# Kernel tuning notes

Measured on AMD Instinct MI355X. Metric: run time of the kernel, lower is better.

Reference implementation:

```python
import jax, jax.numpy as jnp
import numpy as np

N, E, F_IN, G = 50000, 800000, 128, 256
LAYERS = [(128, 4, 64), (256, 4, 64), (256, 1, 64)]  # (fan_in, heads, per-head dim)


def setup_inputs() -> dict:
    key = jax.random.key(0)
    ks = iter(jax.random.split(key, 64))
    nrm = lambda shp, s=1.0: jax.random.normal(next(ks), shp, jnp.float32) * s
    d = {}
    d["x"] = nrm((N, F_IN))
    d["edge_index"] = jax.random.randint(next(ks), (2, E), 0, N, dtype=jnp.int32)
    d["batch"] = jnp.sort(jax.random.randint(next(ks), (N,), 0, G, dtype=jnp.int32))
    for i, (fin, h, c) in enumerate(LAYERS):
        d[f"w{i}"] = nrm((fin, h * c), 1.0 / np.sqrt(fin))
        d[f"asrc{i}"] = nrm((h, c), 0.1)
        d[f"adst{i}"] = nrm((h, c), 0.1)
        d[f"b{i}"] = nrm((h * c,), 0.1)
        d[f"g{i}"] = 1.0 + nrm((h * c,), 0.1)
        d[f"be{i}"] = nrm((h * c,), 0.1)
        d[f"m{i}"] = nrm((h * c,), 0.1)
        d[f"v{i}"] = jnp.abs(nrm((h * c,), 0.1)) + 1.0
    d["fc1w"] = nrm((192, 64), 1.0 / np.sqrt(192)); d["fc1b"] = nrm((64,), 0.1)
    d["fc2w"] = nrm((64, 32), 1.0 / np.sqrt(64));   d["fc2b"] = nrm((32,), 0.1)
    d["fc3w"] = nrm((32, 1), 1.0 / np.sqrt(32));    d["fc3b"] = nrm((1,), 0.1)
    return d


def _gat_layer(x, w, a_s, a_d, b, src, dst, n, heads):
    c = w.shape[1] // heads
    h = (x @ w).reshape(n, heads, c)                      # [N,H,C]
    al_s = jnp.sum(h * a_s[None], axis=-1)                # [N,H]
    al_d = jnp.sum(h * a_d[None], axis=-1)                # [N,H]
    e = jax.nn.leaky_relu(al_s[src] + al_d[dst], 0.2)     # [E',H]
    emax = jax.ops.segment_max(e, dst, num_segments=n)
    emax = jnp.where(jnp.isfinite(emax), emax, 0.0)
    ee = jnp.exp(e - emax[dst])
    den = jax.ops.segment_sum(ee, dst, num_segments=n)
    alpha = ee / (den[dst] + 1e-16)                       # edge softmax per dst node
    out = jax.ops.segment_sum(h[src] * alpha[..., None], dst, num_segments=n)
    return out.reshape(n, heads * c) + b


def _bn(x, g, be, m, v):
    return (x - m) * jax.lax.rsqrt(v + 1e-5) * g + be


def reference(x, edge_index, batch,
              w0, asrc0, adst0, b0, g0, be0, m0, v0,
              w1, asrc1, adst1, b1, g1, be1, m1, v1,
              w2, asrc2, adst2, b2, g2, be2, m2, v2,
              fc1w, fc1b, fc2w, fc2b, fc3w, fc3b):
    n = x.shape[0]
    loop = jnp.arange(n, dtype=edge_index.dtype)          # add_self_loops (PyG default)
    src = jnp.concatenate([edge_index[0], loop])
    dst = jnp.concatenate([edge_index[1], loop])
    layers = [(w0, asrc0, adst0, b0, g0, be0, m0, v0, 4),
              (w1, asrc1, adst1, b1, g1, be1, m1, v1, 4),
              (w2, asrc2, adst2, b2, g2, be2, m2, v2, 1)]
    for (w, a_s, a_d, b, g, be, m, v, heads) in layers:
        x = _gat_layer(x, w, a_s, a_d, b, src, dst, n, heads)
        x = jax.nn.elu(_bn(x, g, be, m, v))
    # multi-pool readout over graphs
    xsum = jax.ops.segment_sum(x, batch, num_segments=G)
    cnt = jax.ops.segment_sum(jnp.ones((n, 1), x.dtype), batch, num_segments=G)
    xmean = xsum / jnp.maximum(cnt, 1.0)
    xmax = jax.ops.segment_max(x, batch, num_segments=G)
    xmax = jnp.where(jnp.isfinite(xmax), xmax, 0.0)
    h = jnp.concatenate([xmean, xmax, xsum], axis=1)      # [G, 192]
    h = jax.nn.relu(h @ fc1w + fc1b)
    h = jax.nn.relu(h @ fc2w + fc2b)
    return h @ fc3w + fc3b                                # [G, 1]
```

## Files before the change

kernel.cpp:

```cpp
#include <hip/hip_runtime.h>
#include <hip/hip_fp16.h>

typedef unsigned short ushort_t;
typedef unsigned int uint_t;
typedef __attribute__((ext_vector_type(8))) _Float16 half8;
typedef __attribute__((ext_vector_type(4))) float f32x4;

#define NN 50000
#define NE 800000
#define NGR 256
#define MAXDEG 64

typedef __attribute__((address_space(3))) unsigned int as3_u32;
typedef const __attribute__((address_space(1))) unsigned int as1_u32c;
__device__ __forceinline__ void gld16(const ushort_t* g, void* lds_base) {
    __builtin_amdgcn_global_load_lds((as1_u32c*)g, (as3_u32*)lds_base, 16, 0, 0);
}

__global__ void k_prep(const float* __restrict__ x0, __half* __restrict__ xf,
                       const float* __restrict__ W0, const float* __restrict__ W1,
                       const float* __restrict__ W2, __half* __restrict__ th,
                       int* __restrict__ colv, int* __restrict__ deg) {
    int i = blockIdx.x * 256 + threadIdx.x;
    if (i < 1600000) {
        float4 v = ((const float4*)x0)[i];
        __half2 a = __floats2half2_rn(v.x, v.y);
        __half2 b = __floats2half2_rn(v.z, v.w);
        *(__half2*)(xf + i * 4) = a;
        *(__half2*)(xf + i * 4 + 2) = b;
    } else if (i < 1600000 + 114688) {
        int w = i - 1600000;
        const float* W; int K, NC, idx, base;
        if (w < 32768)      { W = W0; K = 128; NC = 256; idx = w;         base = 0; }
        else if (w < 98304) { W = W1; K = 256; NC = 256; idx = w - 32768; base = 32768; }
        else                { W = W2; K = 256; NC = 64;  idx = w - 98304; base = 98304; }
        int k = idx / NC, n = idx % NC;
        th[base + n * K + k] = __float2half(W[idx]);
    } else if (i < 1600000 + 114688 + NN) {
        int n = i - 1714688;
        colv[n << 6] = n;
        deg[n] = 1;
    }
}

template<int KD, int BN>
__device__ __forceinline__ void gemm_body(int bx, int by,
    const __half* __restrict__ Ax, const __half* __restrict__ Bth,
    __half* __restrict__ Hout, const float* __restrict__ a_s,
    const float* __restrict__ a_d, float* __restrict__ als,
    float* __restrict__ ald, int H, int M, int NC) {
    constexpr int BM = 128, BK = 32;
    __shared__ ushort_t sA[BM * BK];
    __shared__ ushort_t sB[BN * BK];
    const int tid = threadIdx.x;
    const int m0 = bx * BM;
    const int n0 = by * BN;
    const int wv = tid >> 6, ln = tid & 63;
    const int lrow = ln & 15, lq = ln >> 4;
    constexpr int RT = (BN == 128) ? 4 : 2;
    int wm, wn;
    if constexpr (BN == 128) { wm = (wv >> 1) * 64; wn = (wv & 1) * 64; }
    else                     { wm = wv * 32;        wn = 0; }
    const int roff = ln >> 2;
    const int coff = (ln & 3) * 8;

    f32x4 acc[RT][4] = {};

    for (int k0 = 0; k0 < KD; k0 += BK) {
        #pragma unroll
        for (int ch = 0; ch < 2; ++ch) {
            int rb = wv * 32 + ch * 16;
            size_t ga = (size_t)(m0 + rb + roff) * KD + k0 + coff;
            gld16((const ushort_t*)Ax + ga, &sA[rb * BK]);
        }
        if constexpr (BN == 128) {
            #pragma unroll
            for (int ch = 0; ch < 2; ++ch) {
                int rb = wv * 32 + ch * 16;
                size_t gb = (size_t)(n0 + rb + roff) * KD + k0 + coff;
                gld16((const ushort_t*)Bth + gb, &sB[rb * BK]);
            }
        } else {
            int rb = wv * 16;
            size_t gb = (size_t)(n0 + rb + roff) * KD + k0 + coff;
            gld16((const ushort_t*)Bth + gb, &sB[rb * BK]);
        }
        __syncthreads();
        half8 af[RT], bf[4];
        #pragma unroll
        for (int r = 0; r < RT; ++r)
            af[r] = *(const half8*)&sA[(wm + r * 16 + lrow) * BK + lq * 8];
        #pragma unroll
        for (int c = 0; c < 4; ++c)
            bf[c] = *(const half8*)&sB[(wn + c * 16 + lrow) * BK + lq * 8];
        #pragma unroll
        for (int r = 0; r < RT; ++r)
            #pragma unroll
            for (int c = 0; c < 4; ++c)
                acc[r][c] = __builtin_amdgcn_mfma_f32_16x16x32_f16(af[r], bf[c], acc[r][c], 0, 0, 0);
        __syncthreads();
    }
    #pragma unroll
    for (int r = 0; r < RT; ++r) {
        #pragma unroll
        for (int c = 0; c < 4; ++c) {
            int colg = n0 + wn + c * 16 + lrow;
            #pragma unroll
            for (int j = 0; j < 4; ++j) {
                int row = m0 + wm + r * 16 + lq * 4 + j;
                if (row < M) Hout[(size_t)row * NC + colg] = __float2half(acc[r][c][j]);
            }
        }
    }
    int hh = (n0 + wn) >> 6;
    float asv[4], adv[4];
    #pragma unroll
    for (int c = 0; c < 4; ++c) {
        int cg = (n0 + wn + c * 16 + lrow) & 63;
        asv[c] = a_s[hh * 64 + cg];
        adv[c] = a_d[hh * 64 + cg];
    }
    #pragma unroll
    for (int r = 0; r < RT; ++r) {
        #pragma unroll
        for (int j = 0; j < 4; ++j) {
            float ts = 0.f, td = 0.f;
            #pragma unroll
            for (int c = 0; c < 4; ++c) {
                float v = acc[r][c][j];
                ts += v * asv[c];
                td += v * adv[c];
            }
            #pragma unroll
            for (int m = 1; m < 16; m <<= 1) {
                ts += __shfl_xor(ts, m);
                td += __shfl_xor(td, m);
            }
            int row = m0 + wm + r * 16 + lq * 4 + j;
            if (lrow == 0 && row < M) {
                als[row * H + hh] = ts;
                ald[row * H + hh] = td;
            }
        }
    }
}

template<int KD, int BN>
__global__ __launch_bounds__(256)
void k_mgemm(const __half* __restrict__ Ax, const __half* __restrict__ Bth,
             __half* __restrict__ Hout,
             const float* __restrict__ a_s, const float* __restrict__ a_d,
             float* __restrict__ als, float* __restrict__ ald,
             int H, int M, int NC) {
    gemm_body<KD, BN>(blockIdx.x, blockIdx.y, Ax, Bth, Hout, a_s, a_d, als, ald, H, M, NC);
}

__global__ __launch_bounds__(256)
void k_gf(const __half* __restrict__ Ax, const __half* __restrict__ Bth,
          __half* __restrict__ Hout,
          const float* __restrict__ a_s, const float* __restrict__ a_d,
          float* __restrict__ als, float* __restrict__ ald, int M,
          const int* __restrict__ esrc, const int* __restrict__ edst,
          int* __restrict__ deg, int* __restrict__ colv) {
    if (blockIdx.x < 782) {
        gemm_body<128, 128>(blockIdx.x >> 1, blockIdx.x & 1, Ax, Bth, Hout,
                            a_s, a_d, als, ald, 4, M, 256);
    } else {
        int fid = blockIdx.x - 782;
        int r = blockIdx.x & 7;
        int c = fid >> 3;
        int base = c * 1024 + (int)threadIdx.x * 4;
        if (base < NE) {
            int4 dv = *(const int4*)(edst + base);
            int4 sv = *(const int4*)(esrc + base);
            const int lo = r * 6250;
            const int* dp = (const int*)&dv;
            const int* sp = (const int*)&sv;
            #pragma unroll
            for (int j = 0; j < 4; ++j) {
                int d = dp[j];
                if ((unsigned)(d - lo) < 6250u) {
                    int pos = atomicAdd(&deg[d], 1);
                    if (pos < MAXDEG) colv[(d << 6) + pos] = sp[j];
                }
            }
        }
    }
}

__global__ __launch_bounds__(256)
void k_fagg4s(const __half* __restrict__ h, const float* __restrict__ als,
              const float* __restrict__ ald, const int* __restrict__ deg,
              const int* __restrict__ colv,
              const float* __restrict__ bias, const float* __restrict__ gam,
              const float* __restrict__ bet, const float* __restrict__ mu,
              const float* __restrict__ var,
              __half* __restrict__ xo, int M) {
    __shared__ uint_t wraw[4][64];
    int wv = threadIdx.x >> 6;
    int half = blockIdx.x & 1;
    int node = (blockIdx.x >> 1) * 4 + wv;
    if (node >= M) return;
    int l = threadIdx.x & 63;
    int dg = deg[node];
    int rs = node << 6;

    float2 ad = *(const float2*)(ald + (size_t)node * 4 + half * 2);
    bool vld = l < dg;
    int s = colv[vld ? rs + l : rs];
    int cv = s;
    float2 av = *(const float2*)((const char*)als + ((size_t)(uint_t)s << 4) + half * 8);
    float e0 = av.x + ad.x; e0 = e0 > 0.f ? e0 : 0.2f * e0; e0 = vld ? __expf(e0) : 0.f;
    float e1 = av.y + ad.y; e1 = e1 > 0.f ? e1 : 0.2f * e1; e1 = vld ? __expf(e1) : 0.f;
    float d0 = e0, d1 = e1;
    __half2 p = __floats2half2_rn(e0, e1);
    wraw[wv][l] = *(uint_t*)&p;
    #pragma unroll
    for (int off = 1; off < 64; off <<= 1) {
        d0 += __shfl_xor(d0, off); d1 += __shfl_xor(d1, off);
    }

    float a0 = 0.f, a1 = 0.f;
    const uint_t shB = (uint_t)((l & 32) >> 1);
    const uint_t loffB = (uint_t)(half * 256 + l * 4);
    int nrem = dg;
    #pragma unroll
    for (int grp = 0; grp < 3; ++grp) {
        int g0 = grp * 24;
        if (g0 < nrem) {
            uint_t hu[3][8];
            #pragma unroll
            for (int bb = 0; bb < 3; ++bb) {
                if (g0 + bb * 8 < nrem) {
                    #pragma unroll
                    for (int u = 0; u < 8; ++u) {
                        int sv = __builtin_amdgcn_readlane(cv, g0 + bb * 8 + u);
                        const char* hp = (const char*)h + ((size_t)(uint_t)sv << 9);
                        hu[bb][u] = *(const uint_t*)(hp + loffB);
                    }
                }
            }
            #pragma unroll
            for (int bb = 0; bb < 3; ++bb) {
                if (g0 + bb * 8 < nrem) {
                    #pragma unroll
                    for (int u = 0; u < 8; ++u) {
                        int j = g0 + bb * 8 + u;
                        uint_t w = wraw[wv][j];
                        uint_t afv = w >> shB;
                        asm("v_fma_mix_f32 %0, %1, %2, %0 op_sel:[0,0,0] op_sel_hi:[1,1,0]"
                            : "+v"(a0) : "v"(afv), "v"(hu[bb][u]));
                        asm("v_fma_mix_f32 %0, %1, %2, %0 op_sel:[0,1,0] op_sel_hi:[1,1,0]"
                            : "+v"(a1) : "v"(afv), "v"(hu[bb][u]));
                    }
                }
            }
        }
    }

    float den = (l & 32) ? d1 : d0;
    float inv = 1.f / (den + 1e-16f);
    int chg = half * 128 + l * 2;
    float2 bi = *(const float2*)(bias + chg);
    float2 ga = *(const float2*)(gam + chg);
    float2 be = *(const float2*)(bet + chg);
    float2 m2 = *(const float2*)(mu + chg);
    float2 v2 = *(const float2*)(var + chg);
    float o0 = a0 * inv + bi.x;
    float o1 = a1 * inv + bi.y;
    float bn0 = (o0 - m2.x) * rsqrtf(v2.x + 1e-5f) * ga.x + be.x;
    float bn1 = (o1 - m2.y) * rsqrtf(v2.y + 1e-5f) * ga.y + be.y;
    float f0 = bn0 > 0.f ? bn0 : (__expf(bn0) - 1.f);
    float f1 = bn1 > 0.f ? bn1 : (__expf(bn1) - 1.f);
    __half2 pk = __floats2half2_rn(f0, f1);
    *(uint_t*)&xo[(size_t)node * 256 + chg] = *(uint_t*)&pk;
}

__global__ __launch_bounds__(256)
void k_fagg1(const __half* __restrict__ h, const float* __restrict__ als,
             const float* __restrict__ ald, const int* __restrict__ deg,
             const int* __restrict__ colv,
             const float* __restrict__ bias, const float* __restrict__ gam,
             const float* __restrict__ bet, const float* __restrict__ mu,
             const float* __restrict__ var,
             float* __restrict__ xf, int M) {
    __shared__ uint_t wraw[4][64];
    int node = blockIdx.x * 4 + (threadIdx.x >> 6);
    if (node >= M) return;
    int wv = (threadIdx.x >> 6) & 3;
    int l = threadIdx.x & 63;
    int dg = deg[node];
    int rs = node << 6;

    float ad = ald[node];
    bool vld = l < dg;
    int s = colv[vld ? rs + l : rs];
    int cv = s;
    float e = als[s] + ad; e = e > 0.f ? e : 0.2f * e; e = vld ? __expf(e) : 0.f;
    float d0 = e;
    wraw[wv][l] = __float_as_uint(e);
    #pragma unroll
    for (int off = 1; off < 64; off <<= 1) d0 += __shfl_xor(d0, off);

    float a0 = 0.f;
    int nrem = dg;
    #pragma unroll
    for (int grp = 0; grp < 3; ++grp) {
        int g0 = grp * 24;
        if (g0 < nrem) {
            uint_t hu[3][8];
            #pragma unroll
            for (int bb = 0; bb < 3; ++bb) {
                if (g0 + bb * 8 < nrem) {
                    #pragma unroll
                    for (int u = 0; u < 8; ++u) {
                        int sv = __builtin_amdgcn_readlane(cv, g0 + bb * 8 + u);
                        const ushort_t* hp = (const ushort_t*)h + ((size_t)(uint_t)sv << 6);
                        hu[bb][u] = (uint_t)hp[l];
                    }
                }
            }
            #pragma unroll
            for (int bb = 0; bb < 3; ++bb) {
                if (g0 + bb * 8 < nrem) {
                    #pragma unroll
                    for (int u = 0; u < 8; ++u) {
                        int j = g0 + bb * 8 + u;
                        uint_t wfv = wraw[wv][j];
                        asm("v_fma_mix_f32 %0, %1, %2, %0 op_sel:[0,0,0] op_sel_hi:[0,1,0]"
                            : "+v"(a0) : "v"(wfv), "v"(hu[bb][u]));
                    }
                }
            }
        }
    }

    float inv = 1.f / (d0 + 1e-16f);
    float o = a0 * inv + bias[l];
    float bn = (o - mu[l]) * rsqrtf(var[l] + 1e-5f) * gam[l] + bet[l];
    float fo = bn > 0.f ? bn : (__expf(bn) - 1.f);
    xf[(size_t)node * 64 + l] = fo;
}

__global__ __launch_bounds__(512)
void k_poolfc(const float* __restrict__ x, const int* __restrict__ batch,
              const float* __restrict__ fc1w, const float* __restrict__ fc1b,
              const float* __restrict__ fc2w, const float* __restrict__ fc2b,
              const float* __restrict__ fc3w, const float* __restrict__ fc3b,
              float* __restrict__ out, int M) {
    __shared__ float ssum[8][64];
    __shared__ float smax[8][64];
    __shared__ float hb[192];
    __shared__ float h1[64];
    __shared__ float h2[32];
    int g = blockIdx.x, t = threadIdx.x;
    int d = t & 63, sub = t >> 6;
    int lo = 0, hi = M;
    while (lo < hi) { int mid = (lo + hi) >> 1; if (batch[mid] < g) lo = mid + 1; else hi = mid; }
    int s = lo;
    lo = 0; hi = M;
    while (lo < hi) { int mid = (lo + hi) >> 1; if (batch[mid] < g + 1) lo = mid + 1; else hi = mid; }
    int e = lo;
    float sum = 0.f, mx = -3.0e38f;
    for (int n = s + sub; n < e; n += 8) {
        float v = x[(size_t)n * 64 + d];
        sum += v; mx = fmaxf(mx, v);
    }
    ssum[sub][d] = sum; smax[sub][d] = mx;
    __syncthreads();
    if (t < 64) {
        float sm = 0.f, m2 = -3.0e38f;
        #pragma unroll
        for (int k = 0; k < 8; ++k) { sm += ssum[k][t]; m2 = fmaxf(m2, smax[k][t]); }
        int cnt = e - s;
        hb[t] = sm / (float)(cnt > 1 ? cnt : 1);
        hb[64 + t] = (cnt == 0) ? 0.f : m2;
        hb[128 + t] = sm;
    }
    __syncthreads();
    if (t < 64) {
        float s1 = fc1b[t];
        for (int k = 0; k < 192; ++k) s1 += hb[k] * fc1w[k * 64 + t];
        h1[t] = fmaxf(s1, 0.f);
    }
    __syncthreads();
    if (t < 32) {
        float s2 = fc2b[t];
        for (int k = 0; k < 64; ++k) s2 += h1[k] * fc2w[k * 32 + t];
        h2[t] = fmaxf(s2, 0.f);
    }
    __syncthreads();
    if (t == 0) {
        float s3 = fc3b[0];
        for (int k = 0; k < 32; ++k) s3 += h2[k] * fc3w[k];
        out[g] = s3;
    }
}

extern "C" void kernel_launch(void* const* d_in, const int* in_sizes, int n_in,
                              void* d_out, int out_size, void* d_ws, size_t ws_size,
                              hipStream_t stream) {
    const float* x0     = (const float*)d_in[0];
    const int* ei       = (const int*)d_in[1];
    const int* batch    = (const int*)d_in[2];
    const float* W[3]   = {(const float*)d_in[3],  (const float*)d_in[11], (const float*)d_in[19]};
    const float* AS[3]  = {(const float*)d_in[4],  (const float*)d_in[12], (const float*)d_in[20]};
    const float* AD[3]  = {(const float*)d_in[5],  (const float*)d_in[13], (const float*)d_in[21]};
    const float* BI[3]  = {(const float*)d_in[6],  (const float*)d_in[14], (const float*)d_in[22]};
    const float* GA[3]  = {(const float*)d_in[7],  (const float*)d_in[15], (const float*)d_in[23]};
    const float* BE[3]  = {(const float*)d_in[8],  (const float*)d_in[16], (const float*)d_in[24]};
    const float* MU[3]  = {(const float*)d_in[9],  (const float*)d_in[17], (const float*)d_in[25]};
    const float* VA[3]  = {(const float*)d_in[10], (const float*)d_in[18], (const float*)d_in[26]};
    const float* fc1w = (const float*)d_in[27];
    const float* fc1b = (const float*)d_in[28];
    const float* fc2w = (const float*)d_in[29];
    const float* fc2b = (const float*)d_in[30];
    const float* fc3w = (const float*)d_in[31];
    const float* fc3b = (const float*)d_in[32];

    char* ws = (char*)d_ws;
    int*   colv   = (int*)  (ws);
    int*   deg    = (int*)  (ws + 12800000);
    float* als    = (float*)(ws + 13000192);
    float* ald    = (float*)(ws + 13800192);
    __half* wTh   = (__half*)(ws + 14600192);
    __half* h_buf = (__half*)(ws + 14829568);
    __half* xf16  = (__half*)(ws + 40429568);
    float* xpool  = (float*)(ws + 66054144);

    const int* esrc = ei;
    const int* edst = ei + NE;

    k_prep<<<(1600000 + 114688 + NN + 255) / 256, 256, 0, stream>>>(x0, xf16, W[0], W[1], W[2],
                                                                    wTh, colv, deg);

    const int GB = (NN + 127) / 128;
    const int FILLB = ((NE + 1023) / 1024) * 8;
    int nwb = (NN + 3) / 4;
    int nsb = nwb * 2;

    k_gf<<<782 + FILLB, 256, 0, stream>>>(xf16, wTh, h_buf, AS[0], AD[0], als, ald, NN,
                                          esrc, edst, deg, colv);
    k_fagg4s<<<nsb, 256, 0, stream>>>(h_buf, als, ald, deg, colv,
                                      BI[0], GA[0], BE[0], MU[0], VA[0], xf16, NN);
    k_mgemm<256, 128><<<dim3(GB, 2), 256, 0, stream>>>(xf16, wTh + 32768, h_buf,
                                                       AS[1], AD[1], als, ald, 4, NN, 256);
    k_fagg4s<<<nsb, 256, 0, stream>>>(h_buf, als, ald, deg, colv,
                                      BI[1], GA[1], BE[1], MU[1], VA[1], xf16, NN);
    k_mgemm<256, 64><<<dim3(GB, 1), 256, 0, stream>>>(xf16, wTh + 98304, h_buf,
                                                      AS[2], AD[2], als, ald, 1, NN, 64);
    k_fagg1<<<nwb, 256, 0, stream>>>(h_buf, als, ald, deg, colv,
                                     BI[2], GA[2], BE[2], MU[2], VA[2], xpool, NN);

    k_poolfc<<<NGR, 512, 0, stream>>>(xpool, batch, fc1w, fc1b, fc2w, fc2b, fc3w, fc3b,
                                      (float*)d_out, NN);
    (void)in_sizes; (void)n_in; (void)out_size; (void)ws_size;
}
```

Before: 387.9 us.

## Batch CSR-fill edge loads per thread and dispatch fill blocks before GEMM blocks

New measurement: 384.4 us. No clear change (-0.9%).

```diff
diff --git a/kernel.cpp b/kernel.cpp
--- a/kernel.cpp
+++ b/kernel.cpp
@@ -162,20 +162,30 @@
           float* __restrict__ als, float* __restrict__ ald, int M,
           const int* __restrict__ esrc, const int* __restrict__ edst,
           int* __restrict__ deg, int* __restrict__ colv) {
-    if (blockIdx.x < 782) {
-        gemm_body<128, 128>(blockIdx.x >> 1, blockIdx.x & 1, Ax, Bth, Hout,
+    constexpr int FILLB = ((NE + 4095) / 4096) * 8;
+    if (blockIdx.x >= FILLB) {
+        int g = blockIdx.x - FILLB;
+        gemm_body<128, 128>(g >> 1, g & 1, Ax, Bth, Hout,
                             a_s, a_d, als, ald, 4, M, 256);
     } else {
-        int fid = blockIdx.x - 782;
         int r = blockIdx.x & 7;
-        int c = fid >> 3;
-        int base = c * 1024 + (int)threadIdx.x * 4;
-        if (base < NE) {
-            int4 dv = *(const int4*)(edst + base);
-            int4 sv = *(const int4*)(esrc + base);
-            const int lo = r * 6250;
-            const int* dp = (const int*)&dv;
-            const int* sp = (const int*)&sv;
+        int c = blockIdx.x >> 3;
+        int base = c * 4096 + (int)threadIdx.x * 4;
+        int4 dv[4], sv[4];
+        #pragma unroll
+        for (int u = 0; u < 4; ++u) {
+            int b = base + u * 1024;
+            bool ok = b < NE;
+            int bb = ok ? b : 0;
+            dv[u] = *(const int4*)(edst + bb);
+            sv[u] = *(const int4*)(esrc + bb);
+            if (!ok) { dv[u].x = -1; dv[u].y = -1; dv[u].z = -1; dv[u].w = -1; }
+        }
+        const int lo = r * 6250;
+        #pragma unroll
+        for (int u = 0; u < 4; ++u) {
+            const int* dp = (const int*)&dv[u];
+            const int* sp = (const int*)&sv[u];
             #pragma unroll
             for (int j = 0; j < 4; ++j) {
                 int d = dp[j];
@@ -435,11 +445,11 @@
                                                                     wTh, colv, deg);
 
     const int GB = (NN + 127) / 128;
-    const int FILLB = ((NE + 1023) / 1024) * 8;
+    const int FILLB = ((NE + 4095) / 4096) * 8;
     int nwb = (NN + 3) / 4;
     int nsb = nwb * 2;
 
-    k_gf<<<782 + FILLB, 256, 0, stream>>>(xf16, wTh, h_buf, AS[0], AD[0], als, ald, NN,
+    k_gf<<<FILLB + 782, 256, 0, stream>>>(xf16, wTh, h_buf, AS[0], AD[0], als, ald, NN,
                                           esrc, edst, deg, colv);
     k_fagg4s<<<nsb, 256, 0, stream>>>(h_buf, als, ald, deg, colv,
                                       BI[0], GA[0], BE[0], MU[0], VA[0], xf16, NN);
```
